# Kernel tuning notes

Hardware: AMD Instinct MI355X
Metric: run time of the kernel (lower is better)

Reference implementation:

```python
import jax, jax.numpy as jnp
import numpy as np

N = 50000       # nodes
F_IN = 256
F_OUT = 64
H = 4           # heads
DEG = 16        # avg degree (random edges per node)
NEG_SLOPE = 0.2


def setup_inputs() -> dict:
    key = jax.random.key(0)
    k_h, k_e, k_w, k_fc = jax.random.split(key, 4)
    h = jax.random.normal(k_h, (N, F_IN), dtype=jnp.float32)
    # random edges + explicit self-loops so every node has >= 1 out-edge
    e_rand = jax.random.randint(k_e, (2, N * DEG), 0, N, dtype=jnp.int64)
    loops = jnp.tile(jnp.arange(N, dtype=jnp.int64)[None, :], (2, 1))
    edge_index = jnp.concatenate([e_rand, loops], axis=1)  # [2, 850000]
    # Glorot-uniform-like scales
    s_w = np.sqrt(6.0 / (F_IN + F_OUT)).astype(np.float32)
    s_a = np.sqrt(6.0 / (2 * F_OUT + 1)).astype(np.float32)
    w = jax.random.uniform(k_w, (H, F_IN, F_OUT), jnp.float32, -s_w, s_w)
    fc = jax.random.uniform(k_fc, (H, 2 * F_OUT, 1), jnp.float32, -s_a, s_a)
    bias = jnp.zeros((F_OUT,), jnp.float32)
    return {"h": h, "edge_index": edge_index, "w": w, "fc": fc, "bias": bias}


def reference(h, edge_index, w, fc, bias):
    # GAT forward, vectorized over edges (dropout is identity at inference).
    n = h.shape[0]
    f_out = w.shape[2]
    src, dst = edge_index[0], edge_index[1]           # [E]
    h_prime = jnp.einsum('nf,hfo->hno', h, w)          # [H, N, F]
    a = fc[..., 0]                                     # [H, 2F]
    a_src, a_dst = a[:, :f_out], a[:, f_out:]          # [H, F] each
    s_src = jnp.einsum('hnf,hf->hn', h_prime, a_src)   # [H, N] score of center node
    s_dst = jnp.einsum('hnf,hf->hn', h_prime, a_dst)   # [H, N] score of neighbor
    e = jax.nn.leaky_relu(s_src[:, src] + s_dst[:, dst], NEG_SLOPE)  # [H, E]
    e = e.T                                            # [E, H]
    # segment softmax over edges grouped by source node
    seg_max = jax.ops.segment_max(e, src, num_segments=n)   # [N, H]
    ex = jnp.exp(e - seg_max[src])                           # [E, H]
    denom = jax.ops.segment_sum(ex, src, num_segments=n)    # [N, H]
    alpha = ex / denom[src]                                  # [E, H]
    # scatter-aggregate: out_i = sum_{j in N(i)} alpha_ij * Wh_j
    msgs = alpha[:, :, None] * jnp.transpose(h_prime[:, dst, :], (1, 0, 2))  # [E, H, F]
    out = jax.ops.segment_sum(msgs, src, num_segments=n)    # [N, H, F]
    return out.mean(axis=1) + bias                           # [N, F]
```

## Files before the change

### kernel.cpp

```cpp
#include <hip/hip_runtime.h>
#include <cfloat>

#define FIN 256
#define FOUT 64
#define NH 4
#define NEG_SLOPE 0.2f
#define SLOTS 64

typedef __bf16 bf16x8 __attribute__((ext_vector_type(8)));
typedef float f32x4 __attribute__((ext_vector_type(4)));

__device__ __forceinline__ ushort f2bf(float f) {
    return (ushort)((__float_as_uint(f) + 0x8000u) >> 16);
}
__device__ __forceinline__ float bf2f(ushort u) {
    return __uint_as_float(((unsigned)u) << 16);
}
__device__ __forceinline__ float lrelu(float x) {
    return (x >= 0.f) ? x : NEG_SLOPE * x;
}

__global__ __launch_bounds__(256) void k_pre(const float* __restrict__ w,
                                             ushort* __restrict__ wt)
{
    const int g = blockIdx.x * 256 + threadIdx.x;
    const int hh  = g >> 14;
    const int rem = g & 16383;
    const int col = rem >> 8;
    const int k   = rem & 255;
    wt[g] = f2bf(w[(((hh << 8) | k) << 6) | col]);
}

#define ASTRIDE 280
#define OSTRIDE 260
__global__ __launch_bounds__(256) void k_main(
    const float* __restrict__ h, const ushort* __restrict__ wt,
    const float* __restrict__ fc, ushort* __restrict__ hp,
    float* __restrict__ s_src, float* __restrict__ s_dst, int N,
    const int* __restrict__ ei, int E, int* __restrict__ cursor,
    ushort* __restrict__ col, int scBlocks)
{
    __shared__ ushort Alds[64 * ASTRIDE];

    if ((int)blockIdx.x < scBlocks) {
        const int t = blockIdx.x * 256 + threadIdx.x;
        const int base = t * 8;
        if (base >= E) return;
        if (base + 8 <= E) {
            const int4 s0 = ((const int4*)ei)[t * 2];
            const int4 s1 = ((const int4*)ei)[t * 2 + 1];
            const int4 d0 = ((const int4*)(ei + E))[t * 2];
            const int4 d1 = ((const int4*)(ei + E))[t * 2 + 1];
            const int p0 = atomicAdd(&cursor[s0.x], 1);
            const int p1 = atomicAdd(&cursor[s0.y], 1);
            const int p2 = atomicAdd(&cursor[s0.z], 1);
            const int p3 = atomicAdd(&cursor[s0.w], 1);
            const int p4 = atomicAdd(&cursor[s1.x], 1);
            const int p5 = atomicAdd(&cursor[s1.y], 1);
            const int p6 = atomicAdd(&cursor[s1.z], 1);
            const int p7 = atomicAdd(&cursor[s1.w], 1);
            if (p0 < SLOTS) col[(size_t)s0.x * SLOTS + p0] = (ushort)d0.x;
            if (p1 < SLOTS) col[(size_t)s0.y * SLOTS + p1] = (ushort)d0.y;
            if (p2 < SLOTS) col[(size_t)s0.z * SLOTS + p2] = (ushort)d0.z;
            if (p3 < SLOTS) col[(size_t)s0.w * SLOTS + p3] = (ushort)d0.w;
            if (p4 < SLOTS) col[(size_t)s1.x * SLOTS + p4] = (ushort)d1.x;
            if (p5 < SLOTS) col[(size_t)s1.y * SLOTS + p5] = (ushort)d1.y;
            if (p6 < SLOTS) col[(size_t)s1.z * SLOTS + p6] = (ushort)d1.z;
            if (p7 < SLOTS) col[(size_t)s1.w * SLOTS + p7] = (ushort)d1.w;
        } else {
            for (int e = base; e < E; ++e) {
                const int s = ei[e];
                const int d = ei[E + e];
                const int p = atomicAdd(&cursor[s], 1);
                if (p < SLOTS) col[(size_t)s * SLOTS + p] = (ushort)d;
            }
        }
        return;
    }

    const int bid = blockIdx.x - scBlocks;
    const int tid = threadIdx.x;
    const int n0 = bid * 64;

    for (int idx = tid; idx < 64 * 64; idx += 256) {
        const int row  = idx >> 6;
        const int quad = idx & 63;
        const int n = n0 + row;
        float4 v = make_float4(0.f, 0.f, 0.f, 0.f);
        if (n < N) v = ((const float4*)(h + (size_t)n * FIN))[quad];
        ushort4 b;
        b.x = f2bf(v.x); b.y = f2bf(v.y); b.z = f2bf(v.z); b.w = f2bf(v.w);
        *(ushort4*)&Alds[row * ASTRIDE + quad * 4] = b;
    }
    __syncthreads();

    const int head = tid >> 6;
    const int lane = tid & 63;
    const int lrow = lane & 15;
    const int lq   = lane >> 4;

    const ushort* wth = wt + head * (64 * 256);

    f32x4 acc[4][4];
#pragma unroll
    for (int mt = 0; mt < 4; ++mt)
#pragma unroll
        for (int nt = 0; nt < 4; ++nt)
            acc[mt][nt] = (f32x4){0.f, 0.f, 0.f, 0.f};

#pragma unroll
    for (int kt = 0; kt < 8; ++kt) {
        const int kof = kt * 32 + lq * 8;
        bf16x8 af[4];
#pragma unroll
        for (int mt = 0; mt < 4; ++mt)
            af[mt] = *(const bf16x8*)&Alds[(mt * 16 + lrow) * ASTRIDE + kof];
#pragma unroll
        for (int nt = 0; nt < 4; ++nt) {
            const bf16x8 bfr = *(const bf16x8*)&wth[(nt * 16 + lrow) * 256 + kof];
#pragma unroll
            for (int mt = 0; mt < 4; ++mt)
                acc[mt][nt] = __builtin_amdgcn_mfma_f32_16x16x32_bf16(
                    af[mt], bfr, acc[mt][nt], 0, 0, 0);
        }
    }

    float as_[4], ad_[4];
#pragma unroll
    for (int nt = 0; nt < 4; ++nt) {
        as_[nt] = fc[head * 2 * FOUT + nt * 16 + lrow];
        ad_[nt] = fc[head * 2 * FOUT + FOUT + nt * 16 + lrow];
    }
#pragma unroll
    for (int mt = 0; mt < 4; ++mt) {
        const int rbase = n0 + mt * 16 + lq * 4;
#pragma unroll
        for (int r = 0; r < 4; ++r) {
            const int n = rbase + r;
            float ps = 0.f, pd = 0.f;
#pragma unroll
            for (int nt = 0; nt < 4; ++nt) {
                const float v = acc[mt][nt][r];
                ps = fmaf(v, as_[nt], ps);
                pd = fmaf(v, ad_[nt], pd);
            }
            ps += __shfl_xor(ps, 1); pd += __shfl_xor(pd, 1);
            ps += __shfl_xor(ps, 2); pd += __shfl_xor(pd, 2);
            ps += __shfl_xor(ps, 4); pd += __shfl_xor(pd, 4);
            ps += __shfl_xor(ps, 8); pd += __shfl_xor(pd, 8);
            if (lrow == 0 && n < N) {
                s_src[(size_t)n * NH + head] = ps;
                s_dst[(size_t)n * NH + head] = pd;
            }
        }
    }

    __syncthreads();
#pragma unroll
    for (int mt = 0; mt < 4; ++mt)
#pragma unroll
        for (int r = 0; r < 4; ++r)
#pragma unroll
            for (int nt = 0; nt < 4; ++nt)
                Alds[(mt * 16 + lq * 4 + r) * OSTRIDE +
                     (nt * 16 + lrow) * 4 + head] = f2bf(acc[mt][nt][r]);
    __syncthreads();
    for (int idx = tid; idx < 64 * 64; idx += 256) {
        const int row = idx >> 6;
        const int c   = idx & 63;
        const int n = n0 + row;
        if (n < N)
            *(ushort4*)&hp[(size_t)n * 256 + c * 4] =
                *(const ushort4*)&Alds[row * OSTRIDE + c * 4];
    }
}

__global__ __launch_bounds__(256) void k_agg(
    const int* __restrict__ cursor, const ushort* __restrict__ col,
    const ushort* __restrict__ hp,
    const float* __restrict__ s_src, const float* __restrict__ s_dst,
    const float* __restrict__ bias, float* __restrict__ out, int N, int base)
{
    const int wid  = threadIdx.x >> 6;
    const int lane = threadIdx.x & 63;
    const int n    = base + blockIdx.x * 4 + wid;
    if (n >= N) return;

    const size_t start = (size_t)n * SLOTS;
    const int deg = min(cursor[n], SLOTS);
    const float4 ssn = ((const float4*)s_src)[n];
    const float4* sd4 = (const float4*)s_dst;

    float4 acc = make_float4(0.f, 0.f, 0.f, 0.f);

    int dreg = 0;
    float4 x = make_float4(-FLT_MAX, -FLT_MAX, -FLT_MAX, -FLT_MAX);
    if (lane < deg) {
        dreg = col[start + lane];
        const float4 sd = sd4[dreg];
        x.x = lrelu(ssn.x + sd.x);
        x.y = lrelu(ssn.y + sd.y);
        x.z = lrelu(ssn.z + sd.z);
        x.w = lrelu(ssn.w + sd.w);
    }
    float4 m = x;
#pragma unroll
    for (int d = 32; d; d >>= 1) {
        m.x = fmaxf(m.x, __shfl_xor(m.x, d));
        m.y = fmaxf(m.y, __shfl_xor(m.y, d));
        m.z = fmaxf(m.z, __shfl_xor(m.z, d));
        m.w = fmaxf(m.w, __shfl_xor(m.w, d));
    }
    float4 e = make_float4(0.f, 0.f, 0.f, 0.f);
    if (lane < deg) {
        e.x = __expf(x.x - m.x);
        e.y = __expf(x.y - m.y);
        e.z = __expf(x.z - m.z);
        e.w = __expf(x.w - m.w);
    }
    float4 s = e;
#pragma unroll
    for (int d = 32; d; d >>= 1) {
        s.x += __shfl_xor(s.x, d);
        s.y += __shfl_xor(s.y, d);
        s.z += __shfl_xor(s.z, d);
        s.w += __shfl_xor(s.w, d);
    }
    float4 alpha;
    alpha.x = e.x / s.x;
    alpha.y = e.y / s.y;
    alpha.z = e.z / s.z;
    alpha.w = e.w / s.w;

    const int nblk = (deg + 3) >> 2;
    for (int b = 0; b < nblk; ++b) {
        int dd[4]; float4 av[4]; ushort4 v[4];
#pragma unroll
        for (int u = 0; u < 4; ++u) {
            const int j = b * 4 + u;
            dd[u]   = __shfl(dreg, j);
            av[u].x = __shfl(alpha.x, j);
            av[u].y = __shfl(alpha.y, j);
            av[u].z = __shfl(alpha.z, j);
            av[u].w = __shfl(alpha.w, j);
        }
#pragma unroll
        for (int u = 0; u < 4; ++u)
            v[u] = *(const ushort4*)&hp[((size_t)dd[u] * FOUT + lane) * NH];
#pragma unroll
        for (int u = 0; u < 4; ++u) {
            acc.x = fmaf(av[u].x, bf2f(v[u].x), acc.x);
            acc.y = fmaf(av[u].y, bf2f(v[u].y), acc.y);
            acc.z = fmaf(av[u].z, bf2f(v[u].z), acc.z);
            acc.w = fmaf(av[u].w, bf2f(v[u].w), acc.w);
        }
    }

    out[(size_t)n * FOUT + lane] =
        (acc.x + acc.y + acc.z + acc.w) * 0.25f + bias[lane];
}

extern "C" void kernel_launch(void* const* d_in, const int* in_sizes, int n_in,
                              void* d_out, int out_size, void* d_ws, size_t ws_size,
                              hipStream_t stream)
{
    const float* h    = (const float*)d_in[0];
    const int*   ei   = (const int*)d_in[1];
    const float* w    = (const float*)d_in[2];
    const float* fc   = (const float*)d_in[3];
    const float* bias = (const float*)d_in[4];
    float* out = (float*)d_out;

    const int N = in_sizes[0] / FIN;
    const int E = in_sizes[1] / 2;

    char* ws = (char*)d_ws;
    auto take = [&](size_t bytes) {
        char* p = ws;
        ws += (bytes + 255) & ~(size_t)255;
        return p;
    };
    ushort* wt      = (ushort*)take((size_t)NH * FIN * FOUT * sizeof(ushort));
    ushort* h_prime = (ushort*)take((size_t)NH * N * FOUT * sizeof(ushort));
    float*  s_src   = (float*)take((size_t)NH * N * sizeof(float));
    float*  s_dst   = (float*)take((size_t)NH * N * sizeof(float));
    int*    cursor  = (int*)take((size_t)N * sizeof(int));
    ushort* col     = (ushort*)take((size_t)N * SLOTS * sizeof(ushort));

    hipMemsetAsync(cursor, 0, (size_t)N * sizeof(int), stream);

    k_pre<<<256, 256, 0, stream>>>(w, wt);

    const int scBlocks   = (E / 8 + 255) / 256;
    const int gemmBlocks = (N + 63) / 64;
    k_main<<<scBlocks + gemmBlocks, 256, 0, stream>>>(
        h, wt, fc, h_prime, s_src, s_dst, N, ei, E, cursor, col, scBlocks);

    const int total_blocks = (N + 3) / 4;
    const int hb = total_blocks / 2;
    k_agg<<<hb, 256, 0, stream>>>(cursor, col, h_prime, s_src, s_dst,
                                  bias, out, N, 0);
    k_agg<<<total_blocks - hb, 256, 0, stream>>>(cursor, col, h_prime,
                                                 s_src, s_dst, bias, out, N, hb * 4);
}
```

Measured before the change: 173.4 us.

## Build adjacency lists via two-pass bucketed scatter instead of global atomics

Replaces the per-edge global atomicAdd scatter into per-node slot lists with a two-pass bucket sort. Pass one counts edges per 128-node bucket in LDS, reserves space with one global atomic per bucket, and writes packed (local src, dst) pairs. Pass two assembles each bucket's slot lists in LDS and writes them out coalesced, together with the per-node counts. The aim is to cut random global atomics and scattered 2-byte writes, at the cost of an extra intermediate buffer and a fixed bucket capacity (BCAP) that can silently drop edges if a bucket overflows.

```diff
diff --git a/kernel.cpp b/kernel.cpp
--- a/kernel.cpp
+++ b/kernel.cpp
@@ -6,6 +6,8 @@
 #define NH 4
 #define NEG_SLOPE 0.2f
 #define SLOTS 64
+#define BCAP 3072
+#define P1T 4096
 
 typedef __bf16 bf16x8 __attribute__((ext_vector_type(8)));
 typedef float f32x4 __attribute__((ext_vector_type(4)));
@@ -20,66 +22,100 @@
     return (x >= 0.f) ? x : NEG_SLOPE * x;
 }
 
-__global__ __launch_bounds__(256) void k_pre(const float* __restrict__ w,
-                                             ushort* __restrict__ wt)
+__global__ __launch_bounds__(256) void k1(
+    const int* __restrict__ ei, int E, int nbuck,
+    int* __restrict__ gcur,
+    unsigned* __restrict__ barea,
+    const float* __restrict__ w, ushort* __restrict__ wt, int p1B)
 {
-    const int g = blockIdx.x * 256 + threadIdx.x;
-    const int hh  = g >> 14;
-    const int rem = g & 16383;
-    const int col = rem >> 8;
-    const int k   = rem & 255;
-    wt[g] = f2bf(w[(((hh << 8) | k) << 6) | col]);
+    __shared__ int lcnt[512];
+    __shared__ int lbase[512];
+
+    if ((int)blockIdx.x >= p1B) {
+        const int g = ((int)blockIdx.x - p1B) * 256 + threadIdx.x;
+        const int hh  = g >> 14;
+        const int rem = g & 16383;
+        const int c   = rem >> 8;
+        const int k   = rem & 255;
+        wt[g] = f2bf(w[(((hh << 8) | k) << 6) | c]);
+        return;
+    }
+
+    const int tid = threadIdx.x;
+    for (int b = tid; b < nbuck; b += 256) lcnt[b] = 0;
+    __syncthreads();
+
+    const int e0 = (int)blockIdx.x * P1T;
+    int s[16], d[16];
+#pragma unroll
+    for (int i = 0; i < 16; ++i) {
+        const int e = e0 + i * 256 + tid;
+        if (e < E) {
+            s[i] = ei[e];
+            d[i] = ei[E + e];
+            atomicAdd(&lcnt[s[i] >> 7], 1);
+        } else {
+            s[i] = -1; d[i] = 0;
+        }
+    }
+    __syncthreads();
+    for (int b = tid; b < nbuck; b += 256) {
+        const int c = lcnt[b];
+        lbase[b] = c ? atomicAdd(&gcur[b * 16], c) : 0;
+        lcnt[b] = 0;
+    }
+    __syncthreads();
+#pragma unroll
+    for (int i = 0; i < 16; ++i) {
+        if (s[i] >= 0) {
+            const int b = s[i] >> 7;
+            const int r = atomicAdd(&lcnt[b], 1);
+            const int pos = lbase[b] + r;
+            if (pos < BCAP)
+                barea[(size_t)b * BCAP + pos] =
+                    ((unsigned)(s[i] & 127) << 16) | (unsigned)d[i];
+        }
+    }
 }
 
 #define ASTRIDE 280
 #define OSTRIDE 260
-__global__ __launch_bounds__(256) void k_main(
+__global__ __launch_bounds__(256) void k2(
+    const int* __restrict__ gcur, const unsigned* __restrict__ barea,
+    ushort* __restrict__ col, int* __restrict__ cursor, int p2B,
     const float* __restrict__ h, const ushort* __restrict__ wt,
     const float* __restrict__ fc, ushort* __restrict__ hp,
-    float* __restrict__ s_src, float* __restrict__ s_dst, int N,
-    const int* __restrict__ ei, int E, int* __restrict__ cursor,
-    ushort* __restrict__ col, int scBlocks)
+    float* __restrict__ s_src, float* __restrict__ s_dst, int N)
 {
-    __shared__ ushort Alds[64 * ASTRIDE];
-
-    if ((int)blockIdx.x < scBlocks) {
-        const int t = blockIdx.x * 256 + threadIdx.x;
-        const int base = t * 8;
-        if (base >= E) return;
-        if (base + 8 <= E) {
-            const int4 s0 = ((const int4*)ei)[t * 2];
-            const int4 s1 = ((const int4*)ei)[t * 2 + 1];
-            const int4 d0 = ((const int4*)(ei + E))[t * 2];
-            const int4 d1 = ((const int4*)(ei + E))[t * 2 + 1];
-            const int p0 = atomicAdd(&cursor[s0.x], 1);
-            const int p1 = atomicAdd(&cursor[s0.y], 1);
-            const int p2 = atomicAdd(&cursor[s0.z], 1);
-            const int p3 = atomicAdd(&cursor[s0.w], 1);
-            const int p4 = atomicAdd(&cursor[s1.x], 1);
-            const int p5 = atomicAdd(&cursor[s1.y], 1);
-            const int p6 = atomicAdd(&cursor[s1.z], 1);
-            const int p7 = atomicAdd(&cursor[s1.w], 1);
-            if (p0 < SLOTS) col[(size_t)s0.x * SLOTS + p0] = (ushort)d0.x;
-            if (p1 < SLOTS) col[(size_t)s0.y * SLOTS + p1] = (ushort)d0.y;
-            if (p2 < SLOTS) col[(size_t)s0.z * SLOTS + p2] = (ushort)d0.z;
-            if (p3 < SLOTS) col[(size_t)s0.w * SLOTS + p3] = (ushort)d0.w;
-            if (p4 < SLOTS) col[(size_t)s1.x * SLOTS + p4] = (ushort)d1.x;
-            if (p5 < SLOTS) col[(size_t)s1.y * SLOTS + p5] = (ushort)d1.y;
-            if (p6 < SLOTS) col[(size_t)s1.z * SLOTS + p6] = (ushort)d1.z;
-            if (p7 < SLOTS) col[(size_t)s1.w * SLOTS + p7] = (ushort)d1.w;
-        } else {
-            for (int e = base; e < E; ++e) {
-                const int s = ei[e];
-                const int d = ei[E + e];
-                const int p = atomicAdd(&cursor[s], 1);
-                if (p < SLOTS) col[(size_t)s * SLOTS + p] = (ushort)d;
-            }
-        }
+    __shared__ ushort lds[64 * ASTRIDE];
+
+    const int tid = threadIdx.x;
+
+    if ((int)blockIdx.x < p2B) {
+        ushort* colT = lds;
+        int* cnt = (int*)(lds + 128 * SLOTS);
+        const int b = blockIdx.x;
+        for (int i = tid; i < 128; i += 256) cnt[i] = 0;
+        __syncthreads();
+        int c = gcur[b * 16];
+        if (c > BCAP) c = BCAP;
+        for (int j = tid; j < c; j += 256) {
+            const unsigned p = barea[(size_t)b * BCAP + j];
+            const int sl = (int)(p >> 16);
+            const int r = atomicAdd(&cnt[sl], 1);
+            if (r < SLOTS) colT[sl * SLOTS + r] = (ushort)(p & 0xFFFFu);
+        }
+        __syncthreads();
+        const size_t gbase = (size_t)b * 128 * SLOTS;
+        for (int idx = tid; idx < 128 * SLOTS / 4; idx += 256)
+            *(ushort4*)&col[gbase + (size_t)idx * 4] =
+                *(const ushort4*)&colT[idx * 4];
+        for (int i = tid; i < 128; i += 256)
+            cursor[b * 128 + i] = cnt[i];
         return;
     }
 
-    const int bid = blockIdx.x - scBlocks;
-    const int tid = threadIdx.x;
+    const int bid = (int)blockIdx.x - p2B;
     const int n0 = bid * 64;
 
     for (int idx = tid; idx < 64 * 64; idx += 256) {
@@ -88,9 +124,9 @@
         const int n = n0 + row;
         float4 v = make_float4(0.f, 0.f, 0.f, 0.f);
         if (n < N) v = ((const float4*)(h + (size_t)n * FIN))[quad];
-        ushort4 b;
-        b.x = f2bf(v.x); b.y = f2bf(v.y); b.z = f2bf(v.z); b.w = f2bf(v.w);
-        *(ushort4*)&Alds[row * ASTRIDE + quad * 4] = b;
+        ushort4 bv;
+        bv.x = f2bf(v.x); bv.y = f2bf(v.y); bv.z = f2bf(v.z); bv.w = f2bf(v.w);
+        *(ushort4*)&lds[row * ASTRIDE + quad * 4] = bv;
     }
     __syncthreads();
 
@@ -114,7 +150,7 @@
         bf16x8 af[4];
 #pragma unroll
         for (int mt = 0; mt < 4; ++mt)
-            af[mt] = *(const bf16x8*)&Alds[(mt * 16 + lrow) * ASTRIDE + kof];
+            af[mt] = *(const bf16x8*)&lds[(mt * 16 + lrow) * ASTRIDE + kof];
 #pragma unroll
         for (int nt = 0; nt < 4; ++nt) {
             const bf16x8 bfr = *(const bf16x8*)&wth[(nt * 16 + lrow) * 256 + kof];
@@ -162,8 +198,8 @@
         for (int r = 0; r < 4; ++r)
 #pragma unroll
             for (int nt = 0; nt < 4; ++nt)
-                Alds[(mt * 16 + lq * 4 + r) * OSTRIDE +
-                     (nt * 16 + lrow) * 4 + head] = f2bf(acc[mt][nt][r]);
+                lds[(mt * 16 + lq * 4 + r) * OSTRIDE +
+                    (nt * 16 + lrow) * 4 + head] = f2bf(acc[mt][nt][r]);
     __syncthreads();
     for (int idx = tid; idx < 64 * 64; idx += 256) {
         const int row = idx >> 6;
@@ -171,7 +207,7 @@
         const int n = n0 + row;
         if (n < N)
             *(ushort4*)&hp[(size_t)n * 256 + c * 4] =
-                *(const ushort4*)&Alds[row * OSTRIDE + c * 4];
+                *(const ushort4*)&lds[row * OSTRIDE + c * 4];
     }
 }
 
@@ -273,6 +309,7 @@
 
     const int N = in_sizes[0] / FIN;
     const int E = in_sizes[1] / 2;
+    const int nbuck = (N + 127) >> 7;
 
     char* ws = (char*)d_ws;
     auto take = [&](size_t bytes) {
@@ -280,21 +317,23 @@
         ws += (bytes + 255) & ~(size_t)255;
         return p;
     };
-    ushort* wt      = (ushort*)take((size_t)NH * FIN * FOUT * sizeof(ushort));
-    ushort* h_prime = (ushort*)take((size_t)NH * N * FOUT * sizeof(ushort));
-    float*  s_src   = (float*)take((size_t)NH * N * sizeof(float));
-    float*  s_dst   = (float*)take((size_t)NH * N * sizeof(float));
-    int*    cursor  = (int*)take((size_t)N * sizeof(int));
-    ushort* col     = (ushort*)take((size_t)N * SLOTS * sizeof(ushort));
-
-    hipMemsetAsync(cursor, 0, (size_t)N * sizeof(int), stream);
-
-    k_pre<<<256, 256, 0, stream>>>(w, wt);
-
-    const int scBlocks   = (E / 8 + 255) / 256;
-    const int gemmBlocks = (N + 63) / 64;
-    k_main<<<scBlocks + gemmBlocks, 256, 0, stream>>>(
-        h, wt, fc, h_prime, s_src, s_dst, N, ei, E, cursor, col, scBlocks);
+    ushort*   wt      = (ushort*)take((size_t)NH * FIN * FOUT * sizeof(ushort));
+    ushort*   h_prime = (ushort*)take((size_t)NH * N * FOUT * sizeof(ushort));
+    float*    s_src   = (float*)take((size_t)NH * N * sizeof(float));
+    float*    s_dst   = (float*)take((size_t)NH * N * sizeof(float));
+    int*      cursor  = (int*)take((size_t)nbuck * 128 * sizeof(int));
+    ushort*   col     = (ushort*)take((size_t)nbuck * 128 * SLOTS * sizeof(ushort));
+    int*      gcur    = (int*)take((size_t)nbuck * 16 * sizeof(int));
+    unsigned* barea   = (unsigned*)take((size_t)nbuck * BCAP * sizeof(unsigned));
+
+    hipMemsetAsync(gcur, 0, (size_t)nbuck * 16 * sizeof(int), stream);
+
+    const int p1B = (E + P1T - 1) / P1T;
+    k1<<<p1B + 256, 256, 0, stream>>>(ei, E, nbuck, gcur, barea, w, wt, p1B);
+
+    const int gemmB = (N + 63) / 64;
+    k2<<<nbuck + gemmB, 256, 0, stream>>>(gcur, barea, col, cursor, nbuck,
+                                          h, wt, fc, h_prime, s_src, s_dst, N);
 
     const int total_blocks = (N + 3) / 4;
     const int hb = total_blocks / 2;
```

Measured after the change: 149.9 us. 13.6% less time.
